# Optimization experiments

Hardware: AMD Instinct MI355X
Metric: run time of the kernel (lower is better)

Reference implementation:

```python
import jax, jax.numpy as jnp
import numpy as np

B, N, D = 4096, 64, 128


def setup_inputs() -> dict:
    key = jax.random.key(0)
    ks = jax.random.split(key, 7)
    return {
        "query_emb": jax.random.normal(ks[0], (B, D), jnp.float32),
        "refer_embs": jax.random.normal(ks[1], (B, N, D), jnp.float32),
        "query_r": jax.random.normal(ks[2], (B, D), jnp.float32),
        "refer_r": jax.random.normal(ks[3], (B, N, D), jnp.float32),
        "start_embs": jax.random.normal(ks[4], (B, N, D), jnp.float32),
        "W1": jax.random.normal(ks[5], (D, 2 * D), jnp.float32) * (6.0 / (3 * D)) ** 0.5,  # xavier-ish
        "b1": jnp.zeros((D,), jnp.float32),
        "W2": jax.random.normal(ks[6], (D, D), jnp.float32) * (6.0 / (2 * D)) ** 0.5,
        "b2": jnp.zeros((D,), jnp.float32),
    }


def reference(query_emb, refer_embs, query_r, refer_r, start_embs, W1, b1, W2, b2):
    # bias term per neighbor: [B, N, D]
    bias = refer_embs - start_embs * refer_r
    # broadcast query relation to neighbors and concat -> [B, N, 2D]
    qr = jnp.broadcast_to(query_r[:, None, :], refer_r.shape)
    cat = jnp.concatenate([qr, refer_r], axis=-1)
    h1 = jax.nn.relu(jnp.einsum('bnk,dk->bnd', cat, W1) + b1)
    attn = jnp.einsum('bnk,dk->bnd', h1, W2) + b2
    # weighted sum over neighbor dim -> [B, D]
    final_refer = jnp.sum(attn * bias, axis=-2)
    ref_norm = jnp.sum(jnp.abs(final_refer), axis=-1, keepdims=True)
    query_norm = jnp.sum(jnp.abs(query_emb), axis=-1, keepdims=True)
    const = 2.5
    final_refer = final_refer / (1e-9 + ref_norm / query_norm * const)
    return query_emb + final_refer
```

## Files before the change

### kernel.cpp

```cpp
#include <hip/hip_runtime.h>
#include <hip/hip_bf16.h>


typedef __attribute__((ext_vector_type(8))) short bf16x8;
typedef __attribute__((ext_vector_type(4))) float f32x4;

__device__ __forceinline__ unsigned short f2bf(float x) {
    unsigned int u = __float_as_uint(x);
    u += 0x7FFFu + ((u >> 16) & 1u);
    return (unsigned short)(u >> 16);
}
__device__ __forceinline__ float bf2f(unsigned short h) {
    return __uint_as_float(((unsigned int)h) << 16);
}

__global__ __launch_bounds__(256) void pa_prep(const float* __restrict__ W1,
                                               const float* __restrict__ W2,
                                               unsigned short* __restrict__ w1b,
                                               unsigned short* __restrict__ w2b) {
    int i = blockIdx.x * 256 + threadIdx.x;
    if (i < 16384) {
        int d = i >> 7, k = i & 127;
        w1b[i] = f2bf(W1[d * 256 + 128 + k]);
    } else {
        int j = i - 16384;
        w2b[j] = f2bf(W2[j]);
    }
}

__global__ __launch_bounds__(256) void pa_qv(const float* __restrict__ query_r,
                                             const float* __restrict__ W1,
                                             const float* __restrict__ b1,
                                             float* __restrict__ qv) {
    __shared__ float wa[128][129];
    __shared__ float sq[32][128];
    const int tid = threadIdx.x;
    const int b0 = blockIdx.x * 32;

    for (int i = tid; i < 128 * 128; i += 256) {
        int d = i >> 7, k = i & 127;
        wa[d][k] = W1[d * 256 + k];
    }
    for (int i = tid; i < 32 * 128; i += 256) {
        sq[i >> 7][i & 127] = query_r[(size_t)b0 * 128 + i];
    }
    __syncthreads();

    const int d = tid & 127;
    const int rb = (tid >> 7) * 16;
    const float bb = b1[d];
    for (int j = 0; j < 16; ++j) {
        int r = rb + j;
        float a0 = 0.f, a1 = 0.f, a2 = 0.f, a3 = 0.f;
        #pragma unroll
        for (int k = 0; k < 128; k += 4) {
            a0 += sq[r][k + 0] * wa[d][k + 0];
            a1 += sq[r][k + 1] * wa[d][k + 1];
            a2 += sq[r][k + 2] * wa[d][k + 2];
            a3 += sq[r][k + 3] * wa[d][k + 3];
        }
        qv[(size_t)(b0 + r) * 128 + d] = bb + ((a0 + a1) + (a2 + a3));
    }
}

__global__ __launch_bounds__(256, 4) void pa_main(
    const float* __restrict__ query_emb,
    const float* __restrict__ refer_embs,
    const float* __restrict__ refer_r,
    const float* __restrict__ start_embs,
    const float* __restrict__ qv,
    const unsigned short* __restrict__ w1b,
    const unsigned short* __restrict__ w2b,
    const float* __restrict__ b2,
    float* __restrict__ out) {
    __shared__ __align__(16) unsigned short sR[64 * 128];
    __shared__ __align__(16) unsigned short sH[64 * 128];
    __shared__ float sPart[8][132];
    __shared__ float sQv[128];
    __shared__ float sRed[4];

    const int b    = blockIdx.x;
    const int tid  = threadIdx.x;
    const int lane = tid & 63;
    const int wv   = tid >> 6;
    const int hl   = lane & 15;
    const int qh   = lane >> 4;
    const int wcol = wv * 32;

    const size_t base = (size_t)b * (64 * 128);
    const float4* rr4 = (const float4*)(refer_r + base);
    const float4* re4 = (const float4*)(refer_embs + base);
    const float4* se4 = (const float4*)(start_embs + base);

    float4 rburst[8];
    #pragma unroll
    for (int it = 0; it < 8; ++it) rburst[it] = rr4[tid + it * 256];
    float qvv = (tid < 128) ? qv[(size_t)b * 128 + tid] : 0.f;
    bf16x8 bW[2][4];
    #pragma unroll
    for (int ct = 0; ct < 2; ++ct)
        #pragma unroll
        for (int ks = 0; ks < 4; ++ks)
            bW[ct][ks] = *(const bf16x8*)(w1b + (wcol + ct * 16 + hl) * 128 + ks * 32 + qh * 8);

    if (tid < 128) sQv[tid] = qvv;
    #pragma unroll
    for (int it = 0; it < 8; ++it) {
        int e0  = (tid + it * 256) * 4;
        int row = e0 >> 7;
        int kc  = e0 & 127;
        float4 r = rburst[it];
        ushort4 bv;
        bv.x = f2bf(r.x); bv.y = f2bf(r.y); bv.z = f2bf(r.z); bv.w = f2bf(r.w);
        int byte = row * 256 + ((kc * 2) ^ ((row & 7) << 4));
        *(ushort4*)((char*)sR + byte) = bv;
    }
    __syncthreads();

    f32x4 acc1[4][2] = {};
    #pragma unroll
    for (int rt = 0; rt < 4; ++rt) {
        const int row = rt * 16 + hl;
        const int rsw = (row & 7) << 4;
        bf16x8 af[4];
        #pragma unroll
        for (int ks = 0; ks < 4; ++ks) {
            int byte = row * 256 + ((ks * 64 + qh * 16) ^ rsw);
            af[ks] = *(const bf16x8*)((const char*)sR + byte);
        }
        #pragma unroll
        for (int ct = 0; ct < 2; ++ct)
            #pragma unroll
            for (int ks = 0; ks < 4; ++ks)
                acc1[rt][ct] = __builtin_amdgcn_mfma_f32_16x16x32_bf16(af[ks], bW[ct][ks], acc1[rt][ct], 0, 0, 0);
    }

    #pragma unroll
    for (int ct = 0; ct < 2; ++ct) {
        const int col = wcol + ct * 16 + hl;
        const float q = sQv[col];
        #pragma unroll
        for (int rt = 0; rt < 4; ++rt) {
            #pragma unroll
            for (int j = 0; j < 4; ++j) {
                int row = rt * 16 + qh * 4 + j;
                float h = acc1[rt][ct][j] + q;
                h = h > 0.0f ? h : 0.0f;
                int byte = row * 256 + ((col * 2) ^ ((row & 7) << 4));
                *(unsigned short*)((char*)sH + byte) = f2bf(h);
            }
        }
    }
    __syncthreads();

    bf16x8 bW2[2][4];
    #pragma unroll
    for (int ct = 0; ct < 2; ++ct)
        #pragma unroll
        for (int ks = 0; ks < 4; ++ks)
            bW2[ct][ks] = *(const bf16x8*)(w2b + (wcol + ct * 16 + hl) * 128 + ks * 32 + qh * 8);

    f32x4 acc2[4][2] = {};
    #pragma unroll
    for (int rt = 0; rt < 4; ++rt) {
        const int row = rt * 16 + hl;
        const int rsw = (row & 7) << 4;
        bf16x8 af[4];
        #pragma unroll
        for (int ks = 0; ks < 4; ++ks) {
            int byte = row * 256 + ((ks * 64 + qh * 16) ^ rsw);
            af[ks] = *(const bf16x8*)((const char*)sH + byte);
        }
        #pragma unroll
        for (int ct = 0; ct < 2; ++ct)
            #pragma unroll
            for (int ks = 0; ks < 4; ++ks)
                acc2[rt][ct] = __builtin_amdgcn_mfma_f32_16x16x32_bf16(af[ks], bW2[ct][ks], acc2[rt][ct], 0, 0, 0);
    }

    float4 ge[4], gs[4];
    #pragma unroll
    for (int j = 0; j < 4; ++j) {
        int i = tid + j * 256;
        ge[j] = re4[i];
        gs[j] = se4[i];
    }
    __syncthreads();

    #pragma unroll
    for (int ct = 0; ct < 2; ++ct) {
        const int col = wcol + ct * 16 + hl;
        const float bb = b2[col];
        #pragma unroll
        for (int rt = 0; rt < 4; ++rt) {
            #pragma unroll
            for (int j = 0; j < 4; ++j) {
                int row = rt * 16 + qh * 4 + j;
                int byte = row * 256 + ((col * 2) ^ ((row & 7) << 4));
                *(unsigned short*)((char*)sH + byte) = f2bf(acc2[rt][ct][j] + bb);
            }
        }
    }
    __syncthreads();

    const int t  = tid >> 5;
    const int kc = (tid & 31) * 4;
    float p0 = 0.f, p1 = 0.f, p2 = 0.f, p3 = 0.f;

    #pragma unroll
    for (int j = 0; j < 4; ++j) {
        int i2 = tid + (j + 4) * 256;
        float4 e2 = re4[i2];
        float4 s2 = se4[i2];

        int row  = j * 8 + t;
        int byte = row * 256 + ((kc * 2) ^ ((row & 7) << 4));
        ushort4 a  = *(const ushort4*)((const char*)sH + byte);
        ushort4 rv = *(const ushort4*)((const char*)sR + byte);
        float4 e = ge[j], s = gs[j];
        p0 += bf2f(a.x) * (e.x - s.x * bf2f(rv.x));
        p1 += bf2f(a.y) * (e.y - s.y * bf2f(rv.y));
        p2 += bf2f(a.z) * (e.z - s.z * bf2f(rv.z));
        p3 += bf2f(a.w) * (e.w - s.w * bf2f(rv.w));
        ge[j] = e2; gs[j] = s2;
    }
    #pragma unroll
    for (int j = 0; j < 4; ++j) {
        int row  = (j + 4) * 8 + t;
        int byte = row * 256 + ((kc * 2) ^ ((row & 7) << 4));
        ushort4 a  = *(const ushort4*)((const char*)sH + byte);
        ushort4 rv = *(const ushort4*)((const char*)sR + byte);
        float4 e = ge[j], s = gs[j];
        p0 += bf2f(a.x) * (e.x - s.x * bf2f(rv.x));
        p1 += bf2f(a.y) * (e.y - s.y * bf2f(rv.y));
        p2 += bf2f(a.z) * (e.z - s.z * bf2f(rv.z));
        p3 += bf2f(a.w) * (e.w - s.w * bf2f(rv.w));
    }
    sPart[t][kc + 0] = p0;
    sPart[t][kc + 1] = p1;
    sPart[t][kc + 2] = p2;
    sPart[t][kc + 3] = p3;
    __syncthreads();

    float fv = 0.f, qe = 0.f;
    if (tid < 128) {
        #pragma unroll
        for (int r = 0; r < 8; ++r) fv += sPart[r][tid];
        qe = query_emb[(size_t)b * 128 + tid];
        float rn = fabsf(fv), qn = fabsf(qe);
        #pragma unroll
        for (int off = 1; off < 64; off <<= 1) {
            rn += __shfl_xor(rn, off);
            qn += __shfl_xor(qn, off);
        }
        if (lane == 0) { sRed[wv * 2] = rn; sRed[wv * 2 + 1] = qn; }
    }
    __syncthreads();
    if (tid < 128) {
        float RN = sRed[0] + sRed[2];
        float QN = sRed[1] + sRed[3];
        float scale = 1.0f / (1e-9f + (RN / QN) * 2.5f);
        out[(size_t)b * 128 + tid] = qe + fv * scale;
    }
}

extern "C" void kernel_launch(void* const* d_in, const int* in_sizes, int n_in,
                              void* d_out, int out_size, void* d_ws, size_t ws_size,
                              hipStream_t stream) {
    const float* query_emb  = (const float*)d_in[0];
    const float* refer_embs = (const float*)d_in[1];
    const float* query_r    = (const float*)d_in[2];
    const float* refer_r    = (const float*)d_in[3];
    const float* start_embs = (const float*)d_in[4];
    const float* W1         = (const float*)d_in[5];
    const float* b1         = (const float*)d_in[6];
    const float* W2         = (const float*)d_in[7];
    const float* b2         = (const float*)d_in[8];
    float* out = (float*)d_out;

    char* ws = (char*)d_ws;
    float* qv            = (float*)ws;
    unsigned short* w1b  = (unsigned short*)(ws + 2 * 1024 * 1024);
    unsigned short* w2b  = w1b + 16384;

    pa_prep<<<128, 256, 0, stream>>>(W1, W2, w1b, w2b);
    pa_qv<<<128, 256, 0, stream>>>(query_r, W1, b1, qv);
    pa_main<<<4096, 256, 0, stream>>>(query_emb, refer_embs, refer_r, start_embs,
                                      qv, w1b, w2b, b2, out);
}
```

Baseline: 104.9 us.

## Fold query-relation projection into main kernel via MFMA and hoist neighbor loads

```diff
diff --git a/kernel.cpp b/kernel.cpp
--- a/kernel.cpp
+++ b/kernel.cpp
@@ -16,67 +16,37 @@
 
 __global__ __launch_bounds__(256) void pa_prep(const float* __restrict__ W1,
                                                const float* __restrict__ W2,
+                                               unsigned short* __restrict__ w1a,
                                                unsigned short* __restrict__ w1b,
                                                unsigned short* __restrict__ w2b) {
     int i = blockIdx.x * 256 + threadIdx.x;
+    int j = i & 16383;
+    int d = j >> 7, k = j & 127;
     if (i < 16384) {
-        int d = i >> 7, k = i & 127;
-        w1b[i] = f2bf(W1[d * 256 + 128 + k]);
+        w1a[j] = f2bf(W1[d * 256 + k]);
+    } else if (i < 32768) {
+        w1b[j] = f2bf(W1[d * 256 + 128 + k]);
     } else {
-        int j = i - 16384;
         w2b[j] = f2bf(W2[j]);
     }
 }
 
-__global__ __launch_bounds__(256) void pa_qv(const float* __restrict__ query_r,
-                                             const float* __restrict__ W1,
-                                             const float* __restrict__ b1,
-                                             float* __restrict__ qv) {
-    __shared__ float wa[128][129];
-    __shared__ float sq[32][128];
-    const int tid = threadIdx.x;
-    const int b0 = blockIdx.x * 32;
-
-    for (int i = tid; i < 128 * 128; i += 256) {
-        int d = i >> 7, k = i & 127;
-        wa[d][k] = W1[d * 256 + k];
-    }
-    for (int i = tid; i < 32 * 128; i += 256) {
-        sq[i >> 7][i & 127] = query_r[(size_t)b0 * 128 + i];
-    }
-    __syncthreads();
-
-    const int d = tid & 127;
-    const int rb = (tid >> 7) * 16;
-    const float bb = b1[d];
-    for (int j = 0; j < 16; ++j) {
-        int r = rb + j;
-        float a0 = 0.f, a1 = 0.f, a2 = 0.f, a3 = 0.f;
-        #pragma unroll
-        for (int k = 0; k < 128; k += 4) {
-            a0 += sq[r][k + 0] * wa[d][k + 0];
-            a1 += sq[r][k + 1] * wa[d][k + 1];
-            a2 += sq[r][k + 2] * wa[d][k + 2];
-            a3 += sq[r][k + 3] * wa[d][k + 3];
-        }
-        qv[(size_t)(b0 + r) * 128 + d] = bb + ((a0 + a1) + (a2 + a3));
-    }
-}
-
-__global__ __launch_bounds__(256, 4) void pa_main(
+__global__ __launch_bounds__(256, 2) void pa_main(
     const float* __restrict__ query_emb,
     const float* __restrict__ refer_embs,
+    const float* __restrict__ query_r,
     const float* __restrict__ refer_r,
     const float* __restrict__ start_embs,
-    const float* __restrict__ qv,
+    const unsigned short* __restrict__ w1a,
     const unsigned short* __restrict__ w1b,
     const unsigned short* __restrict__ w2b,
+    const float* __restrict__ b1,
     const float* __restrict__ b2,
     float* __restrict__ out) {
     __shared__ __align__(16) unsigned short sR[64 * 128];
     __shared__ __align__(16) unsigned short sH[64 * 128];
     __shared__ float sPart[8][132];
-    __shared__ float sQv[128];
+    __shared__ __align__(16) unsigned short sQr[128];
     __shared__ float sRed[4];
 
     const int b    = blockIdx.x;
@@ -87,7 +57,7 @@
     const int qh   = lane >> 4;
     const int wcol = wv * 32;
 
-    const size_t base = (size_t)b * (64 * 128);
+    const size_t base = (size_t)b * 8192;
     const float4* rr4 = (const float4*)(refer_r + base);
     const float4* re4 = (const float4*)(refer_embs + base);
     const float4* se4 = (const float4*)(start_embs + base);
@@ -95,15 +65,21 @@
     float4 rburst[8];
     #pragma unroll
     for (int it = 0; it < 8; ++it) rburst[it] = rr4[tid + it * 256];
-    float qvv = (tid < 128) ? qv[(size_t)b * 128 + tid] : 0.f;
-    bf16x8 bW[2][4];
+    float qe   = (tid < 128) ? query_emb[(size_t)b * 128 + tid] : 0.f;
+    float b1v0 = b1[wcol + hl];
+    float b1v1 = b1[wcol + 16 + hl];
+    float b2v0 = b2[wcol + hl];
+    float b2v1 = b2[wcol + 16 + hl];
+    bf16x8 bW[2][4], bWa[2][4];
     #pragma unroll
     for (int ct = 0; ct < 2; ++ct)
         #pragma unroll
-        for (int ks = 0; ks < 4; ++ks)
-            bW[ct][ks] = *(const bf16x8*)(w1b + (wcol + ct * 16 + hl) * 128 + ks * 32 + qh * 8);
-
-    if (tid < 128) sQv[tid] = qvv;
+        for (int ks = 0; ks < 4; ++ks) {
+            bW[ct][ks]  = *(const bf16x8*)(w1b + (wcol + ct * 16 + hl) * 128 + ks * 32 + qh * 8);
+            bWa[ct][ks] = *(const bf16x8*)(w1a + (wcol + ct * 16 + hl) * 128 + ks * 32 + qh * 8);
+        }
+
+    if (tid < 128) sQr[tid] = f2bf(query_r[(size_t)b * 128 + tid]);
     #pragma unroll
     for (int it = 0; it < 8; ++it) {
         int e0  = (tid + it * 256) * 4;
@@ -117,6 +93,33 @@
     }
     __syncthreads();
 
+    bf16x8 bW2[2][4];
+    #pragma unroll
+    for (int ct = 0; ct < 2; ++ct)
+        #pragma unroll
+        for (int ks = 0; ks < 4; ++ks)
+            bW2[ct][ks] = *(const bf16x8*)(w2b + (wcol + ct * 16 + hl) * 128 + ks * 32 + qh * 8);
+    float4 ge[8], gs[8];
+    #pragma unroll
+    for (int j = 0; j < 8; ++j) {
+        int i = tid + j * 256;
+        ge[j] = re4[i];
+        gs[j] = se4[i];
+    }
+
+    f32x4 qvacc[2] = {};
+    {
+        bf16x8 aq[4];
+        #pragma unroll
+        for (int ks = 0; ks < 4; ++ks)
+            aq[ks] = *(const bf16x8*)(sQr + ks * 32 + qh * 8);
+        #pragma unroll
+        for (int ct = 0; ct < 2; ++ct)
+            #pragma unroll
+            for (int ks = 0; ks < 4; ++ks)
+                qvacc[ct] = __builtin_amdgcn_mfma_f32_16x16x32_bf16(aq[ks], bWa[ct][ks], qvacc[ct], 0, 0, 0);
+    }
+
     f32x4 acc1[4][2] = {};
     #pragma unroll
     for (int rt = 0; rt < 4; ++rt) {
@@ -138,13 +141,13 @@
     #pragma unroll
     for (int ct = 0; ct < 2; ++ct) {
         const int col = wcol + ct * 16 + hl;
-        const float q = sQv[col];
+        const float bb = (ct == 0) ? b1v0 : b1v1;
         #pragma unroll
         for (int rt = 0; rt < 4; ++rt) {
             #pragma unroll
             for (int j = 0; j < 4; ++j) {
                 int row = rt * 16 + qh * 4 + j;
-                float h = acc1[rt][ct][j] + q;
+                float h = acc1[rt][ct][j] + qvacc[ct][j] + bb;
                 h = h > 0.0f ? h : 0.0f;
                 int byte = row * 256 + ((col * 2) ^ ((row & 7) << 4));
                 *(unsigned short*)((char*)sH + byte) = f2bf(h);
@@ -153,13 +156,6 @@
     }
     __syncthreads();
 
-    bf16x8 bW2[2][4];
-    #pragma unroll
-    for (int ct = 0; ct < 2; ++ct)
-        #pragma unroll
-        for (int ks = 0; ks < 4; ++ks)
-            bW2[ct][ks] = *(const bf16x8*)(w2b + (wcol + ct * 16 + hl) * 128 + ks * 32 + qh * 8);
-
     f32x4 acc2[4][2] = {};
     #pragma unroll
     for (int rt = 0; rt < 4; ++rt) {
@@ -177,20 +173,12 @@
             for (int ks = 0; ks < 4; ++ks)
                 acc2[rt][ct] = __builtin_amdgcn_mfma_f32_16x16x32_bf16(af[ks], bW2[ct][ks], acc2[rt][ct], 0, 0, 0);
     }
-
-    float4 ge[4], gs[4];
-    #pragma unroll
-    for (int j = 0; j < 4; ++j) {
-        int i = tid + j * 256;
-        ge[j] = re4[i];
-        gs[j] = se4[i];
-    }
     __syncthreads();
 
     #pragma unroll
     for (int ct = 0; ct < 2; ++ct) {
         const int col = wcol + ct * 16 + hl;
-        const float bb = b2[col];
+        const float bb = (ct == 0) ? b2v0 : b2v1;
         #pragma unroll
         for (int rt = 0; rt < 4; ++rt) {
             #pragma unroll
@@ -206,13 +194,8 @@
     const int t  = tid >> 5;
     const int kc = (tid & 31) * 4;
     float p0 = 0.f, p1 = 0.f, p2 = 0.f, p3 = 0.f;
-
-    #pragma unroll
-    for (int j = 0; j < 4; ++j) {
-        int i2 = tid + (j + 4) * 256;
-        float4 e2 = re4[i2];
-        float4 s2 = se4[i2];
-
+    #pragma unroll
+    for (int j = 0; j < 8; ++j) {
         int row  = j * 8 + t;
         int byte = row * 256 + ((kc * 2) ^ ((row & 7) << 4));
         ushort4 a  = *(const ushort4*)((const char*)sH + byte);
@@ -222,19 +205,6 @@
         p1 += bf2f(a.y) * (e.y - s.y * bf2f(rv.y));
         p2 += bf2f(a.z) * (e.z - s.z * bf2f(rv.z));
         p3 += bf2f(a.w) * (e.w - s.w * bf2f(rv.w));
-        ge[j] = e2; gs[j] = s2;
-    }
-    #pragma unroll
-    for (int j = 0; j < 4; ++j) {
-        int row  = (j + 4) * 8 + t;
-        int byte = row * 256 + ((kc * 2) ^ ((row & 7) << 4));
-        ushort4 a  = *(const ushort4*)((const char*)sH + byte);
-        ushort4 rv = *(const ushort4*)((const char*)sR + byte);
-        float4 e = ge[j], s = gs[j];
-        p0 += bf2f(a.x) * (e.x - s.x * bf2f(rv.x));
-        p1 += bf2f(a.y) * (e.y - s.y * bf2f(rv.y));
-        p2 += bf2f(a.z) * (e.z - s.z * bf2f(rv.z));
-        p3 += bf2f(a.w) * (e.w - s.w * bf2f(rv.w));
     }
     sPart[t][kc + 0] = p0;
     sPart[t][kc + 1] = p1;
@@ -242,11 +212,10 @@
     sPart[t][kc + 3] = p3;
     __syncthreads();
 
-    float fv = 0.f, qe = 0.f;
+    float fv = 0.f;
     if (tid < 128) {
         #pragma unroll
         for (int r = 0; r < 8; ++r) fv += sPart[r][tid];
-        qe = query_emb[(size_t)b * 128 + tid];
         float rn = fabsf(fv), qn = fabsf(qe);
         #pragma unroll
         for (int off = 1; off < 64; off <<= 1) {
@@ -278,13 +247,11 @@
     const float* b2         = (const float*)d_in[8];
     float* out = (float*)d_out;
 
-    char* ws = (char*)d_ws;
-    float* qv            = (float*)ws;
-    unsigned short* w1b  = (unsigned short*)(ws + 2 * 1024 * 1024);
-    unsigned short* w2b  = w1b + 16384;
-
-    pa_prep<<<128, 256, 0, stream>>>(W1, W2, w1b, w2b);
-    pa_qv<<<128, 256, 0, stream>>>(query_r, W1, b1, qv);
-    pa_main<<<4096, 256, 0, stream>>>(query_emb, refer_embs, refer_r, start_embs,
-                                      qv, w1b, w2b, b2, out);
-}
+    unsigned short* w1a = (unsigned short*)d_ws;
+    unsigned short* w1b = w1a + 16384;
+    unsigned short* w2b = w1b + 16384;
+
+    pa_prep<<<192, 256, 0, stream>>>(W1, W2, w1a, w1b, w2b);
+    pa_main<<<4096, 256, 0, stream>>>(query_emb, refer_embs, query_r, refer_r,
+                                      start_embs, w1a, w1b, w2b, b1, b2, out);
+}
```

Result: faster. 102.3 us (-2.5%).
